# Kernel tuning notes

Measured on AMD Instinct MI355X. Metric: run time of the kernel, lower is better.

Reference implementation:

```python
import jax, jax.numpy as jnp
import numpy as np

E, N, C, A, S, H, HD, RH = 320000, 20000, 128, 4, 16, 8, 32, 64
AH = H * HD  # 256 attn-head channels; mul_alpha = AH, mul_alpha_head = HD
OUT = 128


def smooth_leaky_relu(x, a=0.2):
    # Equiformer SmoothLeakyReLU: 0.5*((1+a)*x + (1-a)*x*(2*sigmoid(x)-1))
    return 0.5 * ((1 + a) * x + (1 - a) * x * (2.0 * jax.nn.sigmoid(x) - 1.0))


def setup_inputs() -> dict:
    key = jax.random.key(0)
    ks = jax.random.split(key, 20)
    d = {
        'message': jax.random.normal(ks[0], (E, C), jnp.float32),
        'edge_attr': jax.random.normal(ks[1], (E, A), jnp.float32),
        'edge_scalars': jax.random.normal(ks[2], (E, S), jnp.float32),
        'w_rad1': jax.random.normal(ks[3], (S, RH), jnp.float32) / np.sqrt(S),
        'b_rad1': jnp.zeros((RH,), jnp.float32),
        'w_rad2': jax.random.normal(ks[4], (RH, C * A), jnp.float32) / np.sqrt(RH),
        'b_rad2': jnp.zeros((C * A,), jnp.float32),
        'w_dtp_v': jax.random.normal(ks[5], (C, A), jnp.float32) / np.sqrt(A),
        'w_lin_act': jax.random.normal(ks[6], (C, C), jnp.float32) / np.sqrt(C),
        'b_lin_act': jnp.zeros((C,), jnp.float32),
        'w_alpha': jax.random.normal(ks[7], (C, AH), jnp.float32) / np.sqrt(C),
        'b_alpha': jnp.zeros((AH,), jnp.float32),
        'w_lin_v': jax.random.normal(ks[8], (C, AH), jnp.float32) / np.sqrt(C),
        'b_lin_v': jnp.zeros((AH,), jnp.float32),
        'alpha_dot': jax.random.normal(ks[9], (H, HD), jnp.float32) / np.sqrt(HD),
        'w_proj': jax.random.normal(ks[10], (AH, OUT), jnp.float32) / np.sqrt(AH),
        'b_proj': jnp.zeros((OUT,), jnp.float32),
        'edge_dst': jax.random.randint(ks[11], (E,), 0, N, jnp.int32),
        'n_nodes_dst': N,
    }
    return d


def reference(message, edge_attr, edge_scalars,
              w_rad1, b_rad1, w_rad2, b_rad2,
              w_dtp_v, w_lin_act, b_lin_act,
              w_alpha, b_alpha, w_lin_v, b_lin_v,
              alpha_dot, w_proj, b_proj,
              edge_dst, n_nodes_dst):
    n = n_nodes_dst
    # dtp_rad: radial MLP -> per-edge depthwise TP weights [E, C, A]
    h = jax.nn.silu(edge_scalars @ w_rad1 + b_rad1)
    w = (h @ w_rad2 + b_rad2).reshape(-1, C, A)
    # sep_act.dtp (scalar irreps): out[e,c] = msg[e,c] * sum_a w[e,c,a]*attr[e,a]
    msg = message * jnp.einsum('eca,ea->ec', w, edge_attr)
    # sep_alpha -> alpha heads [E, H, HD]
    alpha = (msg @ w_alpha + b_alpha).reshape(-1, H, HD)
    # sep_act.lin + gate (scalars -> SiLU)
    value = jax.nn.silu(msg @ w_lin_act + b_lin_act)
    # sep_value: internal-weight dtp then linear, reshape to heads
    value = value * jnp.einsum('ca,ea->ec', w_dtp_v, edge_attr)
    value = (value @ w_lin_v + b_lin_v).reshape(-1, H, HD)
    # attention logits
    alpha = smooth_leaky_relu(alpha)
    alpha = jnp.einsum('ehk,hk->eh', alpha, alpha_dot)
    # scatter softmax over destination nodes
    amax = jax.ops.segment_max(alpha, edge_dst, num_segments=n)  # [N, H]
    amax = jnp.where(jnp.isfinite(amax), amax, 0.0)
    ex = jnp.exp(alpha - amax[edge_dst])
    denom = jax.ops.segment_sum(ex, edge_dst, num_segments=n)
    alpha = ex / (denom[edge_dst] + 1e-16)
    # weighted scatter-add aggregation
    attn = value * alpha[..., None]  # [E, H, HD]
    node = jax.ops.segment_sum(attn, edge_dst, num_segments=n)  # [N, H, HD]
    node = node.reshape(n, AH)  # heads2vec
    return node @ w_proj + b_proj
```

## Files before the change

kernel.cpp:

```cpp
#include <hip/hip_runtime.h>
#include <hip/hip_bf16.h>

#define C_   128
#define A_   4
#define S_   16
#define RH_  64
#define H_   8
#define AH_  256
#define OUT_ 128

typedef __attribute__((ext_vector_type(8))) short bf16x8;
typedef __attribute__((ext_vector_type(4))) float f32x4;

__device__ __forceinline__ float sigf(float x) { return 1.0f / (1.0f + __expf(-x)); }

__device__ __forceinline__ unsigned short f2bf(float x) {
    unsigned u = __float_as_uint(x);
    unsigned r = (u + 0x7fffu + ((u >> 16) & 1u)) >> 16;
    return (unsigned short)r;
}

__device__ __forceinline__ unsigned pkbf(float a, float b) {
    union { __hip_bfloat162 h; unsigned u; } c;
    c.h = __float22bfloat162_rn(float2{a, b});
    return c.u;
}

__device__ __forceinline__ unsigned enc(float x) {
    unsigned b = __float_as_uint(x);
    return (b & 0x80000000u) ? ~b : (b | 0x80000000u);
}
__device__ __forceinline__ float dec(unsigned u) {
    unsigned b = (u & 0x80000000u) ? (u & 0x7fffffffu) : ~u;
    return __uint_as_float(b);
}

__global__ void k_pack(const float* __restrict__ W, short* __restrict__ out, int K, int N) {
    const int KS = K / 32;
    const int ct = blockIdx.x / KS, ks = blockIdx.x % KS;
    const int l = threadIdx.x, lr = l & 15, lg = l >> 4;
    bf16x8 v;
    #pragma unroll
    for (int j = 0; j < 8; j++)
        v[j] = (short)f2bf(W[(size_t)(ks * 32 + lg * 8 + j) * N + ct * 16 + lr]);
    *(bf16x8*)&out[((size_t)blockIdx.x * 64 + l) * 8] = v;
}

__global__ void k_pack_dtp(const float* __restrict__ W, short* __restrict__ out) {
    const int ct = blockIdx.x >> 3, ks = blockIdx.x & 7;
    const int l = threadIdx.x, lr = l & 15, lg = l >> 4;
    bf16x8 v;
    #pragma unroll
    for (int j = 0; j < 8; j++)
        v[j] = (short)f2bf(W[(size_t)(ks * 8 + lg * 2 + (j >> 2)) * 512 + (ct * 16 + lr) * 4 + (j & 3)]);
    *(bf16x8*)&out[((size_t)blockIdx.x * 64 + l) * 8] = v;
}

__global__ __launch_bounds__(256) void k_hist(
    const int* __restrict__ edge_dst, int* __restrict__ deg, int E)
{
    const int e = blockIdx.x * 256 + threadIdx.x;
    if (e < E) atomicAdd(&deg[edge_dst[e]], 1);
}

__global__ __launch_bounds__(1024) void k_scan(
    const int* __restrict__ deg, int* __restrict__ base, int* __restrict__ cursor, int N)
{
    __shared__ int part[1024];
    const int t = threadIdx.x;
    const int per = (N + 1023) / 1024;
    const int i0 = t * per;
    int s = 0;
    for (int i = 0; i < per; i++) { int idx = i0 + i; if (idx < N) s += deg[idx]; }
    part[t] = s;
    __syncthreads();
    for (int off = 1; off < 1024; off <<= 1) {
        int v = (t >= off) ? part[t - off] : 0;
        __syncthreads();
        part[t] += v;
        __syncthreads();
    }
    int excl = (t == 0) ? 0 : part[t - 1];
    for (int i = 0; i < per; i++) {
        int idx = i0 + i;
        if (idx < N) { base[idx] = excl; cursor[idx] = excl; excl += deg[idx]; }
    }
}

__global__ __launch_bounds__(256) void k_fill(
    const int* __restrict__ edge_dst, int* __restrict__ cursor,
    int* __restrict__ sorted, int E)
{
    const int e = blockIdx.x * 256 + threadIdx.x;
    if (e < E) {
        const int pos = atomicAdd(&cursor[edge_dst[e]], 1);
        sorted[pos] = e;
    }
}

__global__ __launch_bounds__(512, 4) void k_msgalpha(
    const float* __restrict__ message, const float* __restrict__ edge_attr,
    const float* __restrict__ edge_scalars,
    const float* __restrict__ w_rad1, const float* __restrict__ b_rad1,
    const short* __restrict__ w_rad2_lin, const float* __restrict__ b_rad2,
    const short* __restrict__ w_alpha_lin, const float* __restrict__ b_alpha,
    const float* __restrict__ alpha_dot, const int* __restrict__ edge_dst,
    short* __restrict__ msg_bf, float* __restrict__ logits, unsigned* __restrict__ amax_u)
{
    __shared__ __align__(16) char smem[50432];
    short* Ap     = (short*)smem;
    short* msg_s  = (short*)(smem + 32768);
    float* w1_s   = (float*)(smem + 32768);
    float* es_s   = (float*)(smem + 32768 + 4096);
    float* attr_s = (float*)(smem + 49152);
    int*   dst_s  = (int*)(smem + 50176);

    const int t = threadIdx.x;
    const long e0 = (long)blockIdx.x * 64;

    if (t < 256) {
        *(float4*)&w1_s[t * 4] = *(const float4*)&w_rad1[t * 4];
    } else {
        const int i = t - 256, r = i >> 2, s4 = (i & 3) * 4;
        *(float4*)&es_s[r * 17 + s4] = *(const float4*)&edge_scalars[(e0 + r) * S_ + s4];
    }
    if (t < 64) {
        *(float4*)&attr_s[t * 4] = *(const float4*)&edge_attr[(e0 + t) * A_];
        dst_s[t] = edge_dst[e0 + t];
    }
    __syncthreads();

    {
        const int r = t & 63, o0 = (t >> 6) * 8;
        float acc[8];
        #pragma unroll
        for (int i = 0; i < 8; i++) acc[i] = b_rad1[o0 + i];
        #pragma unroll
        for (int s = 0; s < S_; s++) {
            const float ev = es_s[r * 17 + s];
            #pragma unroll
            for (int i = 0; i < 8; i++) acc[i] += ev * w1_s[s * 64 + o0 + i];
        }
        float h[8];
        #pragma unroll
        for (int i = 0; i < 8; i++) { const float x = acc[i]; h[i] = x * sigf(x); }
        const float4 a4 = *(const float4*)&attr_s[r * 4];
        char* base = (char*)Ap + r * 512;
        const int sw = (r & 31) << 4;
        #pragma unroll
        for (int c = 0; c < 4; c++) {
            const float h0 = h[2 * c], h1 = h[2 * c + 1];
            uint4 v;
            v.x = pkbf(h0 * a4.x, h0 * a4.y);
            v.y = pkbf(h0 * a4.z, h0 * a4.w);
            v.z = pkbf(h1 * a4.x, h1 * a4.y);
            v.w = pkbf(h1 * a4.z, h1 * a4.w);
            *(uint4*)(base + ((o0 * 8 + c * 16) ^ sw)) = v;
        }
    }
    __syncthreads();

    const int w = t >> 6, l = t & 63, lr = l & 15, lg = l >> 4;

    {
        bf16x8 bf[8];
        #pragma unroll
        for (int ks = 0; ks < 8; ks++)
            bf[ks] = *(const bf16x8*)&w_rad2_lin[((size_t)(w * 8 + ks) * 64 + l) * 8];
        const int col = w * 16 + lr;
        const float4 b2 = *(const float4*)&b_rad2[col * 4];
        #pragma unroll 1
        for (int rt = 0; rt < 4; rt++) {
            const int arow = rt * 16 + lr;
            const char* abase = (char*)Ap + arow * 512;
            const int asw = (arow & 31) << 4;
            bf16x8 af[8];
            #pragma unroll
            for (int ks = 0; ks < 8; ks++)
                af[ks] = *(const bf16x8*)(abase + ((ks * 64 + lg * 16) ^ asw));
            f32x4 acc = {0.f, 0.f, 0.f, 0.f};
            #pragma unroll
            for (int ks = 0; ks < 8; ks++)
                acc = __builtin_amdgcn_mfma_f32_16x16x32_bf16(af[ks], bf[ks], acc, 0, 0, 0);
            #pragma unroll
            for (int r = 0; r < 4; r++) {
                const int row = rt * 16 + lg * 4 + r;
                const float4 a4 = *(const float4*)&attr_s[row * 4];
                const float badj = a4.x * b2.x + a4.y * b2.y + a4.z * b2.z + a4.w * b2.w;
                const float m = message[(e0 + row) * C_ + col];
                *(short*)((char*)msg_s + row * 256 + ((col * 2) ^ ((row & 15) << 4))) =
                    (short)f2bf(m * (acc[r] + badj));
            }
        }
    }
    __syncthreads();

    {
        #pragma unroll
        for (int i = 0; i < 2; i++) {
            const int q = t + i * 512;
            const int row = q >> 4, ch = q & 15;
            const uint4 v = *(const uint4*)((char*)msg_s + row * 256 + ((ch * 16) ^ ((row & 15) << 4)));
            *(uint4*)((char*)msg_bf + ((e0 + row) * 256 + ch * 16)) = v;
        }
    }

    {
        bf16x8 waf[2][4];
        float4 ba4[2], ad4[2];
        #pragma unroll
        for (int q = 0; q < 2; q++) {
            const int rt = w * 2 + q;
            #pragma unroll
            for (int ks = 0; ks < 4; ks++)
                waf[q][ks] = *(const bf16x8*)&w_alpha_lin[((size_t)(rt * 4 + ks) * 64 + l) * 8];
            ba4[q] = *(const float4*)&b_alpha[rt * 16 + lg * 4];
            ad4[q] = *(const float4*)&alpha_dot[rt * 16 + lg * 4];
        }
        #pragma unroll 1
        for (int ct = 0; ct < 4; ct++) {
            const int erow = ct * 16 + lr;
            const char* mbase = (char*)msg_s + erow * 256;
            const int msw = (erow & 15) << 4;
            bf16x8 mb[4];
            #pragma unroll
            for (int ks = 0; ks < 4; ks++)
                mb[ks] = *(const bf16x8*)(mbase + ((ks * 64 + lg * 16) ^ msw));
            float s = 0.f;
            #pragma unroll
            for (int q = 0; q < 2; q++) {
                f32x4 acc = {0.f, 0.f, 0.f, 0.f};
                #pragma unroll
                for (int ks = 0; ks < 4; ks++)
                    acc = __builtin_amdgcn_mfma_f32_16x16x32_bf16(waf[q][ks], mb[ks], acc, 0, 0, 0);
                #pragma unroll
                for (int r = 0; r < 4; r++) {
                    const float x = acc[r] + ((const float*)&ba4[q])[r];
                    const float y = x * (0.2f + 0.8f * sigf(x));
                    s += y * ((const float*)&ad4[q])[r];
                }
            }
            s += __shfl_xor(s, 16);
            s += __shfl_xor(s, 32);
            if (lg == 0) {
                const long e = e0 + ct * 16 + lr;
                logits[e * H_ + w] = s;
                atomicMax(&amax_u[dst_s[ct * 16 + lr] * H_ + w], enc(s));
            }
        }
    }
}

__global__ __launch_bounds__(256) void k_denom(
    const float* __restrict__ logits, const int* __restrict__ edge_dst,
    const unsigned* __restrict__ amax_u, float* __restrict__ denom, int EH)
{
    const int t = blockIdx.x * 256 + threadIdx.x;
    if (t >= EH) return;
    const int e = t >> 3, h = t & 7;
    const int n = edge_dst[e];
    const float am = dec(amax_u[n * H_ + h]);
    atomicAdd(&denom[n * H_ + h], __expf(logits[t] - am));
}

__global__ __launch_bounds__(512, 2) void k_value(
    const short* __restrict__ msg_bf, const float* __restrict__ edge_attr,
    const short* __restrict__ w_lin_act_lin, const float* __restrict__ b_lin_act,
    const float* __restrict__ w_dtp_v,
    const short* __restrict__ w_lin_v_lin, const float* __restrict__ b_lin_v,
    const float* __restrict__ logits, const int* __restrict__ edge_dst,
    const unsigned* __restrict__ amax_u, const float* __restrict__ denom,
    const int* __restrict__ sorted, float* __restrict__ node)
{
    __shared__ __align__(16) char pool[66560];
    __shared__ float attr_s[64][4];
    __shared__ float wgt_s[64][H_];
    __shared__ int   dst_s[64];
    __shared__ int   eid_s[64];
    short* a_s  = (short*)pool;
    short* v_s  = (short*)(pool + 16384);
    float* val2 = (float*)pool;

    const int t = threadIdx.x;
    const int b0 = blockIdx.x * 64;

    if (t < 64) {
        const int e = sorted[b0 + t];
        eid_s[t] = e;
        dst_s[t] = edge_dst[e];
        *(float4*)&attr_s[t][0] = *(const float4*)&edge_attr[(long)e * A_];
    }
    __syncthreads();
    #pragma unroll
    for (int i = 0; i < 2; i++) {
        const int q = t + i * 512;
        const int row = q >> 4, ch = q & 15;
        const uint4 v = *(const uint4*)((const char*)msg_bf + ((long)eid_s[row] * 256 + ch * 16));
        *(uint4*)((char*)a_s + row * 256 + ((ch * 16) ^ ((row & 15) << 4))) = v;
    }
    {
        const int el = t >> 3, h = t & 7;
        const long e = eid_s[el];
        const int n = dst_s[el];
        const float am = dec(amax_u[n * H_ + h]);
        const float d  = denom[n * H_ + h];
        wgt_s[el][h] = __expf(logits[e * H_ + h] - am) / (d + 1e-16f);
    }
    __syncthreads();

    const int w = t >> 6, l = t & 63, lr = l & 15, lg = l >> 4;
    {
        bf16x8 af[4][4];
        #pragma unroll
        for (int rt = 0; rt < 4; rt++)
            #pragma unroll
            for (int ks = 0; ks < 4; ks++) {
                const int row = rt * 16 + lr;
                af[rt][ks] = *(bf16x8*)((char*)a_s + row * 256 + ((ks * 64 + lg * 16) ^ ((row & 15) << 4)));
            }
        bf16x8 bf[4];
        #pragma unroll
        for (int ks = 0; ks < 4; ks++)
            bf[ks] = *(const bf16x8*)&w_lin_act_lin[((size_t)(w * 4 + ks) * 64 + l) * 8];
        const int col = w * 16 + lr;
        const float bb = b_lin_act[col];
        const float4 wv = *(const float4*)&w_dtp_v[col * 4];
        #pragma unroll
        for (int rt = 0; rt < 4; rt++) {
            f32x4 acc = {0.f, 0.f, 0.f, 0.f};
            #pragma unroll
            for (int ks = 0; ks < 4; ks++)
                acc = __builtin_amdgcn_mfma_f32_16x16x32_bf16(af[rt][ks], bf[ks], acc, 0, 0, 0);
            #pragma unroll
            for (int r = 0; r < 4; r++) {
                const int row = rt * 16 + lg * 4 + r;
                float x = acc[r] + bb;
                x = x * sigf(x);
                const float4 a4 = *(const float4*)&attr_s[row][0];
                const float dv = wv.x * a4.x + wv.y * a4.y + wv.z * a4.z + wv.w * a4.w;
                *(short*)((char*)v_s + row * 256 + ((col * 2) ^ ((row & 15) << 4))) =
                    (short)f2bf(x * dv);
            }
        }
    }
    __syncthreads();

    bf16x8 vf[4][4];
    #pragma unroll
    for (int rt = 0; rt < 4; rt++)
        #pragma unroll
        for (int ks = 0; ks < 4; ks++) {
            const int row = rt * 16 + lr;
            vf[rt][ks] = *(bf16x8*)((char*)v_s + row * 256 + ((ks * 64 + lg * 16) ^ ((row & 15) << 4)));
        }
    __syncthreads();

    #pragma unroll
    for (int q = 0; q < 2; q++) {
        const int ct = w * 2 + q;
        bf16x8 bf[4];
        #pragma unroll
        for (int ks = 0; ks < 4; ks++)
            bf[ks] = *(const bf16x8*)&w_lin_v_lin[((size_t)(ct * 4 + ks) * 64 + l) * 8];
        const int col = ct * 16 + lr;
        const float bb = b_lin_v[col];
        #pragma unroll
        for (int rt = 0; rt < 4; rt++) {
            f32x4 acc = {0.f, 0.f, 0.f, 0.f};
            #pragma unroll
            for (int ks = 0; ks < 4; ks++)
                acc = __builtin_amdgcn_mfma_f32_16x16x32_bf16(vf[rt][ks], bf[ks], acc, 0, 0, 0);
            #pragma unroll
            for (int r = 0; r < 4; r++) {
                const int row = rt * 16 + lg * 4 + r;
                val2[row * 260 + col] = (acc[r] + bb) * wgt_s[row][col >> 5];
            }
        }
    }
    __syncthreads();
    {
        const int c = t & 255, eS = (t >> 8) * 32, eE = eS + 32;
        float run = 0.f;
        int s = eS;
        #pragma unroll 1
        for (int e = eS; e < eE; e++) {
            run += val2[e * 260 + c];
            const bool end = (e == eE - 1) || (dst_s[e + 1] != dst_s[e]);
            if (end) {
                float* np = node + (long)dst_s[e] * AH_ + c;
                if (s == eS || e == eE - 1) atomicAdd(np, run);
                else *np = run;
                run = 0.f; s = e + 1;
            }
        }
    }
}

__global__ __launch_bounds__(256) void k_proj(
    const float* __restrict__ node, const float* __restrict__ w_proj,
    const float* __restrict__ b_proj, float* __restrict__ out)
{
    __shared__ float node_s[32][AH_];
    const int t = threadIdx.x;
    const long n0 = (long)blockIdx.x * 32;
    #pragma unroll
    for (int i = 0; i < 8; i++) {
        const int idx = t + i * 256;
        const int nl = idx >> 6, c4 = (idx & 63) * 4;
        *(float4*)&node_s[nl][c4] = *(const float4*)&node[(n0 + nl) * AH_ + c4];
    }
    __syncthreads();
    const int j0 = (t & 31) * 4;
    const int g  = t >> 5;
    float4 acc4[4];
    const float4 b = *(const float4*)&b_proj[j0];
    #pragma unroll
    for (int i = 0; i < 4; i++) acc4[i] = b;
    const float* wp = w_proj + j0;
    for (int c4 = 0; c4 < 64; c4++) {
        const float4 w0 = *(const float4*)&wp[(c4 * 4 + 0) * OUT_];
        const float4 w1 = *(const float4*)&wp[(c4 * 4 + 1) * OUT_];
        const float4 w2 = *(const float4*)&wp[(c4 * 4 + 2) * OUT_];
        const float4 w3 = *(const float4*)&wp[(c4 * 4 + 3) * OUT_];
        #pragma unroll
        for (int i = 0; i < 4; i++) {
            const float4 nv = *(const float4*)&node_s[g * 4 + i][c4 * 4];
            acc4[i].x += nv.x * w0.x + nv.y * w1.x + nv.z * w2.x + nv.w * w3.x;
            acc4[i].y += nv.x * w0.y + nv.y * w1.y + nv.z * w2.y + nv.w * w3.y;
            acc4[i].z += nv.x * w0.z + nv.y * w1.z + nv.z * w2.z + nv.w * w3.z;
            acc4[i].w += nv.x * w0.w + nv.y * w1.w + nv.z * w2.w + nv.w * w3.w;
        }
    }
    #pragma unroll
    for (int i = 0; i < 4; i++) {
        const long n = n0 + g * 4 + i;
        *(float4*)&out[n * OUT_ + j0] = acc4[i];
    }
}

extern "C" void kernel_launch(void* const* d_in, const int* in_sizes, int n_in,
                              void* d_out, int out_size, void* d_ws, size_t ws_size,
                              hipStream_t stream)
{
    const float* message      = (const float*)d_in[0];
    const float* edge_attr    = (const float*)d_in[1];
    const float* edge_scalars = (const float*)d_in[2];
    const float* w_rad1       = (const float*)d_in[3];
    const float* b_rad1       = (const float*)d_in[4];
    const float* w_rad2       = (const float*)d_in[5];
    const float* b_rad2       = (const float*)d_in[6];
    const float* w_dtp_v      = (const float*)d_in[7];
    const float* w_lin_act    = (const float*)d_in[8];
    const float* b_lin_act    = (const float*)d_in[9];
    const float* w_alpha      = (const float*)d_in[10];
    const float* b_alpha      = (const float*)d_in[11];
    const float* w_lin_v      = (const float*)d_in[12];
    const float* b_lin_v      = (const float*)d_in[13];
    const float* alpha_dot    = (const float*)d_in[14];
    const float* w_proj       = (const float*)d_in[15];
    const float* b_proj       = (const float*)d_in[16];
    const int*   edge_dst     = (const int*)d_in[17];

    const int E = in_sizes[0] / C_;
    const int N = out_size / OUT_;

    char* ws = (char*)d_ws;
    float*    node     = (float*)ws;
    unsigned* amax_u   = (unsigned*)(node + (size_t)N * AH_);
    float*    denom    = (float*)(amax_u + (size_t)N * H_);
    int*      deg      = (int*)(denom + (size_t)N * H_);
    int*      base     = deg + N;
    int*      cursor   = base + N;
    int*      sorted   = cursor + N;
    short*    w_rad2_l = (short*)(sorted + E);
    short*    w_alph_l = w_rad2_l + 64 * 512;
    short*    w_lact_l = w_alph_l + 128 * 256;
    short*    w_linv_l = w_lact_l + 128 * 128;
    short*    msg_bf   = w_linv_l + 128 * 256;
    float*    logits   = (float*)(msg_bf + (size_t)E * C_);

    hipMemsetAsync(d_ws, 0, (size_t)N * (AH_ + 2 * H_ + 1) * 4, stream);

    const int nbE256 = (E + 255) / 256;
    k_pack_dtp<<<64, 64, 0, stream>>>(w_rad2, w_rad2_l);
    k_pack<<<(256/16)*(128/32), 64, 0, stream>>>(w_alpha,   w_alph_l, 128, 256);
    k_pack<<<(128/16)*(128/32), 64, 0, stream>>>(w_lin_act, w_lact_l, 128, 128);
    k_pack<<<(256/16)*(128/32), 64, 0, stream>>>(w_lin_v,   w_linv_l, 128, 256);
    k_hist<<<nbE256, 256, 0, stream>>>(edge_dst, deg, E);
    k_scan<<<1, 1024, 0, stream>>>(deg, base, cursor, N);
    k_fill<<<nbE256, 256, 0, stream>>>(edge_dst, cursor, sorted, E);
    k_msgalpha<<<E / 64, 512, 0, stream>>>(message, edge_attr, edge_scalars,
                                           w_rad1, b_rad1, w_rad2_l, b_rad2,
                                           w_alph_l, b_alpha, alpha_dot, edge_dst,
                                           msg_bf, logits, amax_u);
    k_denom<<<(E * H_ + 255) / 256, 256, 0, stream>>>(logits, edge_dst, amax_u, denom, E * H_);
    k_value<<<E / 64, 512, 0, stream>>>(msg_bf, edge_attr, w_lact_l, b_lin_act, w_dtp_v,
                                        w_linv_l, b_lin_v, logits, edge_dst, amax_u, denom,
                                        sorted, node);
    k_proj<<<N / 32, 256, 0, stream>>>(node, w_proj, b_proj, (float*)d_out);
}
```

Baseline: 420.1 us.

## Scatter msg and logit records into dst-sorted order in producer kernel

Instead of a sorted edge-index list that k_value later gathers through, k_fill now computes each edge's rank and k_msgalpha writes msg and a packed per-edge record (logits, bf16 attr, dst) straight to the sorted position. k_value then reads contiguous rows, and k_denom pre-reduces runs of equal destinations over 8 sorted edges before its atomics. k_msgalpha is also reshaped to 32 edges and 256 threads per block for higher occupancy. The cost moves to scattered writes in the producer, and edge_attr in the value path is now rounded to bf16.

```diff
diff --git a/kernel.cpp b/kernel.cpp
--- a/kernel.cpp
+++ b/kernel.cpp
@@ -25,6 +25,8 @@
     c.h = __float22bfloat162_rn(float2{a, b});
     return c.u;
 }
+__device__ __forceinline__ float bflo(unsigned u) { return __uint_as_float(u << 16); }
+__device__ __forceinline__ float bfhi(unsigned u) { return __uint_as_float(u & 0xffff0000u); }
 
 __device__ __forceinline__ unsigned enc(float x) {
     unsigned b = __float_as_uint(x);
@@ -64,7 +66,7 @@
 }
 
 __global__ __launch_bounds__(1024) void k_scan(
-    const int* __restrict__ deg, int* __restrict__ base, int* __restrict__ cursor, int N)
+    const int* __restrict__ deg, int* __restrict__ cursor, int N)
 {
     __shared__ int part[1024];
     const int t = threadIdx.x;
@@ -83,61 +85,64 @@
     int excl = (t == 0) ? 0 : part[t - 1];
     for (int i = 0; i < per; i++) {
         int idx = i0 + i;
-        if (idx < N) { base[idx] = excl; cursor[idx] = excl; excl += deg[idx]; }
+        if (idx < N) { cursor[idx] = excl; excl += deg[idx]; }
     }
 }
 
 __global__ __launch_bounds__(256) void k_fill(
     const int* __restrict__ edge_dst, int* __restrict__ cursor,
-    int* __restrict__ sorted, int E)
+    int* __restrict__ rank, int E)
 {
     const int e = blockIdx.x * 256 + threadIdx.x;
-    if (e < E) {
-        const int pos = atomicAdd(&cursor[edge_dst[e]], 1);
-        sorted[pos] = e;
-    }
-}
-
-__global__ __launch_bounds__(512, 4) void k_msgalpha(
+    if (e < E) rank[e] = atomicAdd(&cursor[edge_dst[e]], 1);
+}
+
+__global__ __launch_bounds__(256, 6) void k_msgalpha(
     const float* __restrict__ message, const float* __restrict__ edge_attr,
     const float* __restrict__ edge_scalars,
     const float* __restrict__ w_rad1, const float* __restrict__ b_rad1,
     const short* __restrict__ w_rad2_lin, const float* __restrict__ b_rad2,
     const short* __restrict__ w_alpha_lin, const float* __restrict__ b_alpha,
     const float* __restrict__ alpha_dot, const int* __restrict__ edge_dst,
-    short* __restrict__ msg_bf, float* __restrict__ logits, unsigned* __restrict__ amax_u)
-{
-    __shared__ __align__(16) char smem[50432];
+    const int* __restrict__ rank,
+    short* __restrict__ msg_srt, float* __restrict__ rec_srt, unsigned* __restrict__ amax_u)
+{
+    __shared__ __align__(16) char smem[26624];
     short* Ap     = (short*)smem;
-    short* msg_s  = (short*)(smem + 32768);
-    float* w1_s   = (float*)(smem + 32768);
-    float* es_s   = (float*)(smem + 32768 + 4096);
-    float* attr_s = (float*)(smem + 49152);
-    int*   dst_s  = (int*)(smem + 50176);
+    short* msg_s  = (short*)(smem + 16384);
+    float* w1_s   = (float*)(smem + 16384);
+    float* es_t   = (float*)(smem + 16384 + 4096);
+    float* attr_s = (float*)(smem + 24576);
+    float* rec_s  = (float*)(smem + 25088);
 
     const int t = threadIdx.x;
-    const long e0 = (long)blockIdx.x * 64;
-
-    if (t < 256) {
-        *(float4*)&w1_s[t * 4] = *(const float4*)&w_rad1[t * 4];
-    } else {
-        const int i = t - 256, r = i >> 2, s4 = (i & 3) * 4;
-        *(float4*)&es_s[r * 17 + s4] = *(const float4*)&edge_scalars[(e0 + r) * S_ + s4];
-    }
-    if (t < 64) {
-        *(float4*)&attr_s[t * 4] = *(const float4*)&edge_attr[(e0 + t) * A_];
-        dst_s[t] = edge_dst[e0 + t];
-    }
-    __syncthreads();
-
-    {
-        const int r = t & 63, o0 = (t >> 6) * 8;
+    const long e0 = (long)blockIdx.x * 32;
+
+    *(float4*)&w1_s[t * 4] = *(const float4*)&w_rad1[t * 4];
+    if (t < 128) {
+        const int r = t >> 2, s4 = (t & 3) * 4;
+        const float4 v = *(const float4*)&edge_scalars[(e0 + r) * S_ + s4];
+        es_t[(s4 + 0) * 32 + r] = v.x; es_t[(s4 + 1) * 32 + r] = v.y;
+        es_t[(s4 + 2) * 32 + r] = v.z; es_t[(s4 + 3) * 32 + r] = v.w;
+    }
+    if (t < 32) {
+        const float4 a = *(const float4*)&edge_attr[(e0 + t) * A_];
+        *(float4*)&attr_s[t * 4] = a;
+        rec_s[t * 12 + 8]  = __uint_as_float(pkbf(a.x, a.y));
+        rec_s[t * 12 + 9]  = __uint_as_float(pkbf(a.z, a.w));
+        rec_s[t * 12 + 10] = __int_as_float(edge_dst[e0 + t]);
+        rec_s[t * 12 + 11] = 0.f;
+    }
+    __syncthreads();
+
+    {
+        const int r = t & 31, o0 = (t >> 5) * 8;
         float acc[8];
         #pragma unroll
         for (int i = 0; i < 8; i++) acc[i] = b_rad1[o0 + i];
         #pragma unroll
         for (int s = 0; s < S_; s++) {
-            const float ev = es_s[r * 17 + s];
+            const float ev = es_t[s * 32 + r];
             #pragma unroll
             for (int i = 0; i < 8; i++) acc[i] += ev * w1_s[s * 64 + o0 + i];
         }
@@ -163,120 +168,143 @@
     const int w = t >> 6, l = t & 63, lr = l & 15, lg = l >> 4;
 
     {
-        bf16x8 bf[8];
-        #pragma unroll
-        for (int ks = 0; ks < 8; ks++)
-            bf[ks] = *(const bf16x8*)&w_rad2_lin[((size_t)(w * 8 + ks) * 64 + l) * 8];
-        const int col = w * 16 + lr;
-        const float4 b2 = *(const float4*)&b_rad2[col * 4];
-        #pragma unroll 1
-        for (int rt = 0; rt < 4; rt++) {
-            const int arow = rt * 16 + lr;
-            const char* abase = (char*)Ap + arow * 512;
-            const int asw = (arow & 31) << 4;
-            bf16x8 af[8];
+        #pragma unroll
+        for (int q = 0; q < 2; q++) {
+            const int ct = w * 2 + q;
+            bf16x8 bf[8];
             #pragma unroll
             for (int ks = 0; ks < 8; ks++)
-                af[ks] = *(const bf16x8*)(abase + ((ks * 64 + lg * 16) ^ asw));
-            f32x4 acc = {0.f, 0.f, 0.f, 0.f};
-            #pragma unroll
-            for (int ks = 0; ks < 8; ks++)
-                acc = __builtin_amdgcn_mfma_f32_16x16x32_bf16(af[ks], bf[ks], acc, 0, 0, 0);
-            #pragma unroll
-            for (int r = 0; r < 4; r++) {
-                const int row = rt * 16 + lg * 4 + r;
-                const float4 a4 = *(const float4*)&attr_s[row * 4];
-                const float badj = a4.x * b2.x + a4.y * b2.y + a4.z * b2.z + a4.w * b2.w;
-                const float m = message[(e0 + row) * C_ + col];
-                *(short*)((char*)msg_s + row * 256 + ((col * 2) ^ ((row & 15) << 4))) =
-                    (short)f2bf(m * (acc[r] + badj));
-            }
-        }
-    }
-    __syncthreads();
-
-    {
-        #pragma unroll
-        for (int i = 0; i < 2; i++) {
-            const int q = t + i * 512;
-            const int row = q >> 4, ch = q & 15;
-            const uint4 v = *(const uint4*)((char*)msg_s + row * 256 + ((ch * 16) ^ ((row & 15) << 4)));
-            *(uint4*)((char*)msg_bf + ((e0 + row) * 256 + ch * 16)) = v;
-        }
-    }
-
-    {
-        bf16x8 waf[2][4];
-        float4 ba4[2], ad4[2];
-        #pragma unroll
-        for (int q = 0; q < 2; q++) {
-            const int rt = w * 2 + q;
-            #pragma unroll
-            for (int ks = 0; ks < 4; ks++)
-                waf[q][ks] = *(const bf16x8*)&w_alpha_lin[((size_t)(rt * 4 + ks) * 64 + l) * 8];
-            ba4[q] = *(const float4*)&b_alpha[rt * 16 + lg * 4];
-            ad4[q] = *(const float4*)&alpha_dot[rt * 16 + lg * 4];
-        }
-        #pragma unroll 1
-        for (int ct = 0; ct < 4; ct++) {
-            const int erow = ct * 16 + lr;
-            const char* mbase = (char*)msg_s + erow * 256;
-            const int msw = (erow & 15) << 4;
-            bf16x8 mb[4];
-            #pragma unroll
-            for (int ks = 0; ks < 4; ks++)
-                mb[ks] = *(const bf16x8*)(mbase + ((ks * 64 + lg * 16) ^ msw));
-            float s = 0.f;
-            #pragma unroll
-            for (int q = 0; q < 2; q++) {
+                bf[ks] = *(const bf16x8*)&w_rad2_lin[((size_t)(ct * 8 + ks) * 64 + l) * 8];
+            const int col = ct * 16 + lr;
+            const float4 b2 = *(const float4*)&b_rad2[col * 4];
+            #pragma unroll
+            for (int rt = 0; rt < 2; rt++) {
+                const int arow = rt * 16 + lr;
+                const char* abase = (char*)Ap + arow * 512;
+                const int asw = (arow & 31) << 4;
+                bf16x8 af[8];
+                #pragma unroll
+                for (int ks = 0; ks < 8; ks++)
+                    af[ks] = *(const bf16x8*)(abase + ((ks * 64 + lg * 16) ^ asw));
                 f32x4 acc = {0.f, 0.f, 0.f, 0.f};
                 #pragma unroll
-                for (int ks = 0; ks < 4; ks++)
-                    acc = __builtin_amdgcn_mfma_f32_16x16x32_bf16(waf[q][ks], mb[ks], acc, 0, 0, 0);
+                for (int ks = 0; ks < 8; ks++)
+                    acc = __builtin_amdgcn_mfma_f32_16x16x32_bf16(af[ks], bf[ks], acc, 0, 0, 0);
                 #pragma unroll
                 for (int r = 0; r < 4; r++) {
-                    const float x = acc[r] + ((const float*)&ba4[q])[r];
-                    const float y = x * (0.2f + 0.8f * sigf(x));
-                    s += y * ((const float*)&ad4[q])[r];
+                    const int row = rt * 16 + lg * 4 + r;
+                    const float4 a4 = *(const float4*)&attr_s[row * 4];
+                    const float badj = a4.x * b2.x + a4.y * b2.y + a4.z * b2.z + a4.w * b2.w;
+                    const float m = message[(e0 + row) * C_ + col];
+                    *(short*)((char*)msg_s + row * 256 + ((col * 2) ^ ((row & 15) << 4))) =
+                        (short)f2bf(m * (acc[r] + badj));
                 }
             }
-            s += __shfl_xor(s, 16);
-            s += __shfl_xor(s, 32);
-            if (lg == 0) {
-                const long e = e0 + ct * 16 + lr;
-                logits[e * H_ + w] = s;
-                atomicMax(&amax_u[dst_s[ct * 16 + lr] * H_ + w], enc(s));
+        }
+    }
+    __syncthreads();
+
+    {
+        #pragma unroll
+        for (int i = 0; i < 2; i++) {
+            const int q = t + i * 256;
+            const int row = q >> 4, lc = q & 15;
+            const int rk = rank[e0 + row];
+            const uint4 v = *(const uint4*)((char*)msg_s + row * 256 + ((lc * 16) ^ ((row & 15) << 4)));
+            *(uint4*)((char*)msg_srt + (size_t)rk * 256 + ((lc * 16) ^ ((rk & 15) << 4))) = v;
+        }
+    }
+
+    {
+        #pragma unroll
+        for (int hq = 0; hq < 2; hq++) {
+            const int hd = w * 2 + hq;
+            bf16x8 waf[2][4];
+            float4 ba4[2], ad4[2];
+            #pragma unroll
+            for (int q = 0; q < 2; q++) {
+                const int ctw = hd * 2 + q;
+                #pragma unroll
+                for (int ks = 0; ks < 4; ks++)
+                    waf[q][ks] = *(const bf16x8*)&w_alpha_lin[((size_t)(ctw * 4 + ks) * 64 + l) * 8];
+                ba4[q] = *(const float4*)&b_alpha[ctw * 16 + lg * 4];
+                ad4[q] = *(const float4*)&alpha_dot[ctw * 16 + lg * 4];
             }
-        }
+            #pragma unroll
+            for (int ct = 0; ct < 2; ct++) {
+                const int erow = ct * 16 + lr;
+                const char* mbase = (char*)msg_s + erow * 256;
+                const int msw = (erow & 15) << 4;
+                bf16x8 mb[4];
+                #pragma unroll
+                for (int ks = 0; ks < 4; ks++)
+                    mb[ks] = *(const bf16x8*)(mbase + ((ks * 64 + lg * 16) ^ msw));
+                float s = 0.f;
+                #pragma unroll
+                for (int q = 0; q < 2; q++) {
+                    f32x4 acc = {0.f, 0.f, 0.f, 0.f};
+                    #pragma unroll
+                    for (int ks = 0; ks < 4; ks++)
+                        acc = __builtin_amdgcn_mfma_f32_16x16x32_bf16(waf[q][ks], mb[ks], acc, 0, 0, 0);
+                    #pragma unroll
+                    for (int r = 0; r < 4; r++) {
+                        const float x = acc[r] + ((const float*)&ba4[q])[r];
+                        const float y = x * (0.2f + 0.8f * sigf(x));
+                        s += y * ((const float*)&ad4[q])[r];
+                    }
+                }
+                s += __shfl_xor(s, 16);
+                s += __shfl_xor(s, 32);
+                if (lg == 0) {
+                    rec_s[(ct * 16 + lr) * 12 + hd] = s;
+                    const int n = edge_dst[e0 + ct * 16 + lr];
+                    atomicMax(&amax_u[n * H_ + hd], enc(s));
+                }
+            }
+        }
+    }
+    __syncthreads();
+
+    if (t < 96) {
+        const int e = t / 3, ch = t % 3;
+        const int rk = rank[e0 + e];
+        *(float4*)&rec_srt[(size_t)rk * 12 + ch * 4] = *(const float4*)&rec_s[e * 12 + ch * 4];
     }
 }
 
 __global__ __launch_bounds__(256) void k_denom(
-    const float* __restrict__ logits, const int* __restrict__ edge_dst,
-    const unsigned* __restrict__ amax_u, float* __restrict__ denom, int EH)
-{
-    const int t = blockIdx.x * 256 + threadIdx.x;
-    if (t >= EH) return;
-    const int e = t >> 3, h = t & 7;
-    const int n = edge_dst[e];
-    const float am = dec(amax_u[n * H_ + h]);
-    atomicAdd(&denom[n * H_ + h], __expf(logits[t] - am));
+    const float* __restrict__ rec_srt, const unsigned* __restrict__ amax_u,
+    float* __restrict__ denom, int E)
+{
+    const int idx = blockIdx.x * 256 + threadIdx.x;
+    if (idx >= E) return;
+    const int c8 = idx >> 3, h = idx & 7;
+    const float* rp = rec_srt + (size_t)c8 * 96;
+    int nprev = -1; float run = 0.f, am = 0.f;
+    #pragma unroll 1
+    for (int e = 0; e < 8; e++) {
+        const int n = __float_as_int(rp[e * 12 + 10]);
+        if (n != nprev) {
+            if (nprev >= 0) atomicAdd(&denom[nprev * H_ + h], run);
+            nprev = n; run = 0.f;
+            am = dec(amax_u[n * H_ + h]);
+        }
+        run += __expf(rp[e * 12 + h] - am);
+    }
+    atomicAdd(&denom[nprev * H_ + h], run);
 }
 
 __global__ __launch_bounds__(512, 2) void k_value(
-    const short* __restrict__ msg_bf, const float* __restrict__ edge_attr,
+    const short* __restrict__ msg_srt,
     const short* __restrict__ w_lin_act_lin, const float* __restrict__ b_lin_act,
     const float* __restrict__ w_dtp_v,
     const short* __restrict__ w_lin_v_lin, const float* __restrict__ b_lin_v,
-    const float* __restrict__ logits, const int* __restrict__ edge_dst,
-    const unsigned* __restrict__ amax_u, const float* __restrict__ denom,
-    const int* __restrict__ sorted, float* __restrict__ node)
+    const float* __restrict__ rec_srt, const unsigned* __restrict__ amax_u,
+    const float* __restrict__ denom, float* __restrict__ node)
 {
     __shared__ __align__(16) char pool[66560];
-    __shared__ float attr_s[64][4];
+    __shared__ float rec_s[64 * 12];
     __shared__ float wgt_s[64][H_];
-    __shared__ int   dst_s[64];
-    __shared__ int   eid_s[64];
     short* a_s  = (short*)pool;
     short* v_s  = (short*)(pool + 16384);
     float* val2 = (float*)pool;
@@ -284,60 +312,54 @@
     const int t = threadIdx.x;
     const int b0 = blockIdx.x * 64;
 
-    if (t < 64) {
-        const int e = sorted[b0 + t];
-        eid_s[t] = e;
-        dst_s[t] = edge_dst[e];
-        *(float4*)&attr_s[t][0] = *(const float4*)&edge_attr[(long)e * A_];
-    }
-    __syncthreads();
     #pragma unroll
     for (int i = 0; i < 2; i++) {
         const int q = t + i * 512;
-        const int row = q >> 4, ch = q & 15;
-        const uint4 v = *(const uint4*)((const char*)msg_bf + ((long)eid_s[row] * 256 + ch * 16));
-        *(uint4*)((char*)a_s + row * 256 + ((ch * 16) ^ ((row & 15) << 4))) = v;
-    }
+        *(uint4*)((char*)a_s + q * 16) =
+            *(const uint4*)((const char*)msg_srt + (size_t)b0 * 256 + q * 16);
+    }
+    if (t < 192) {
+        const int e = t / 3, ch = t % 3;
+        *(float4*)&rec_s[e * 12 + ch * 4] =
+            *(const float4*)&rec_srt[(size_t)(b0 + e) * 12 + ch * 4];
+    }
+    __syncthreads();
     {
         const int el = t >> 3, h = t & 7;
-        const long e = eid_s[el];
-        const int n = dst_s[el];
+        const int n = __float_as_int(rec_s[el * 12 + 10]);
         const float am = dec(amax_u[n * H_ + h]);
         const float d  = denom[n * H_ + h];
-        wgt_s[el][h] = __expf(logits[e * H_ + h] - am) / (d + 1e-16f);
-    }
-    __syncthreads();
+        wgt_s[el][h] = __expf(rec_s[el * 12 + h] - am) / (d + 1e-16f);
+    }
 
     const int w = t >> 6, l = t & 63, lr = l & 15, lg = l >> 4;
     {
-        bf16x8 af[4][4];
-        #pragma unroll
-        for (int rt = 0; rt < 4; rt++)
-            #pragma unroll
-            for (int ks = 0; ks < 4; ks++) {
-                const int row = rt * 16 + lr;
-                af[rt][ks] = *(bf16x8*)((char*)a_s + row * 256 + ((ks * 64 + lg * 16) ^ ((row & 15) << 4)));
-            }
-        bf16x8 bf[4];
+        bf16x8 bfg[4];
         #pragma unroll
         for (int ks = 0; ks < 4; ks++)
-            bf[ks] = *(const bf16x8*)&w_lin_act_lin[((size_t)(w * 4 + ks) * 64 + l) * 8];
+            bfg[ks] = *(const bf16x8*)&w_lin_act_lin[((size_t)(w * 4 + ks) * 64 + l) * 8];
         const int col = w * 16 + lr;
         const float bb = b_lin_act[col];
         const float4 wv = *(const float4*)&w_dtp_v[col * 4];
         #pragma unroll
         for (int rt = 0; rt < 4; rt++) {
+            const int arow = rt * 16 + lr;
+            bf16x8 af[4];
+            #pragma unroll
+            for (int ks = 0; ks < 4; ks++)
+                af[ks] = *(bf16x8*)((char*)a_s + arow * 256 + ((ks * 64 + lg * 16) ^ ((arow & 15) << 4)));
             f32x4 acc = {0.f, 0.f, 0.f, 0.f};
             #pragma unroll
             for (int ks = 0; ks < 4; ks++)
-                acc = __builtin_amdgcn_mfma_f32_16x16x32_bf16(af[rt][ks], bf[ks], acc, 0, 0, 0);
+                acc = __builtin_amdgcn_mfma_f32_16x16x32_bf16(af[ks], bfg[ks], acc, 0, 0, 0);
             #pragma unroll
             for (int r = 0; r < 4; r++) {
                 const int row = rt * 16 + lg * 4 + r;
                 float x = acc[r] + bb;
                 x = x * sigf(x);
-                const float4 a4 = *(const float4*)&attr_s[row][0];
-                const float dv = wv.x * a4.x + wv.y * a4.y + wv.z * a4.z + wv.w * a4.w;
+                const unsigned u0 = __float_as_uint(rec_s[row * 12 + 8]);
+                const unsigned u1 = __float_as_uint(rec_s[row * 12 + 9]);
+                const float dv = wv.x * bflo(u0) + wv.y * bfhi(u0) + wv.z * bflo(u1) + wv.w * bfhi(u1);
                 *(short*)((char*)v_s + row * 256 + ((col * 2) ^ ((row & 15) << 4))) =
                     (short)f2bf(x * dv);
             }
@@ -385,9 +407,10 @@
         #pragma unroll 1
         for (int e = eS; e < eE; e++) {
             run += val2[e * 260 + c];
-            const bool end = (e == eE - 1) || (dst_s[e + 1] != dst_s[e]);
+            const int de = __float_as_int(rec_s[e * 12 + 10]);
+            const bool end = (e == eE - 1) || (__float_as_int(rec_s[(e + 1) * 12 + 10]) != de);
             if (end) {
-                float* np = node + (long)dst_s[e] * AH_ + c;
+                float* np = node + (long)de * AH_ + c;
                 if (s == eS || e == eE - 1) atomicAdd(np, run);
                 else *np = run;
                 run = 0.f; s = e + 1;
@@ -469,15 +492,14 @@
     unsigned* amax_u   = (unsigned*)(node + (size_t)N * AH_);
     float*    denom    = (float*)(amax_u + (size_t)N * H_);
     int*      deg      = (int*)(denom + (size_t)N * H_);
-    int*      base     = deg + N;
-    int*      cursor   = base + N;
-    int*      sorted   = cursor + N;
-    short*    w_rad2_l = (short*)(sorted + E);
+    int*      cursor   = deg + N;
+    int*      rank     = cursor + N;
+    short*    w_rad2_l = (short*)(rank + E);
     short*    w_alph_l = w_rad2_l + 64 * 512;
     short*    w_lact_l = w_alph_l + 128 * 256;
     short*    w_linv_l = w_lact_l + 128 * 128;
-    short*    msg_bf   = w_linv_l + 128 * 256;
-    float*    logits   = (float*)(msg_bf + (size_t)E * C_);
+    short*    msg_srt  = w_linv_l + 128 * 256;
+    float*    rec_srt  = (float*)(msg_srt + (size_t)E * C_);
 
     hipMemsetAsync(d_ws, 0, (size_t)N * (AH_ + 2 * H_ + 1) * 4, stream);
 
@@ -487,15 +509,14 @@
     k_pack<<<(128/16)*(128/32), 64, 0, stream>>>(w_lin_act, w_lact_l, 128, 128);
     k_pack<<<(256/16)*(128/32), 64, 0, stream>>>(w_lin_v,   w_linv_l, 128, 256);
     k_hist<<<nbE256, 256, 0, stream>>>(edge_dst, deg, E);
-    k_scan<<<1, 1024, 0, stream>>>(deg, base, cursor, N);
-    k_fill<<<nbE256, 256, 0, stream>>>(edge_dst, cursor, sorted, E);
-    k_msgalpha<<<E / 64, 512, 0, stream>>>(message, edge_attr, edge_scalars,
+    k_scan<<<1, 1024, 0, stream>>>(deg, cursor, N);
+    k_fill<<<nbE256, 256, 0, stream>>>(edge_dst, cursor, rank, E);
+    k_msgalpha<<<E / 32, 256, 0, stream>>>(message, edge_attr, edge_scalars,
                                            w_rad1, b_rad1, w_rad2_l, b_rad2,
-                                           w_alph_l, b_alpha, alpha_dot, edge_dst,
-                                           msg_bf, logits, amax_u);
-    k_denom<<<(E * H_ + 255) / 256, 256, 0, stream>>>(logits, edge_dst, amax_u, denom, E * H_);
-    k_value<<<E / 64, 512, 0, stream>>>(msg_bf, edge_attr, w_lact_l, b_lin_act, w_dtp_v,
-                                        w_linv_l, b_lin_v, logits, edge_dst, amax_u, denom,
-                                        sorted, node);
+                                           w_alph_l, b_alpha, alpha_dot, edge_dst, rank,
+                                           msg_srt, rec_srt, amax_u);
+    k_denom<<<nbE256, 256, 0, stream>>>(rec_srt, amax_u, denom, E);
+    k_value<<<E / 64, 512, 0, stream>>>(msg_srt, w_lact_l, b_lin_act, w_dtp_v,
+                                        w_linv_l, b_lin_v, rec_srt, amax_u, denom, node);
     k_proj<<<N / 32, 256, 0, stream>>>(node, w_proj, b_proj, (float*)d_out);
 }
```

Result: slower. 543.3 us (+29.3%).

## Shrink msgalpha to 32-edge blocks of 256 threads and trim k_value register use

Applied to the files above, without the earlier changes.

k_msgalpha now processes 32 edges per block with 256 threads (4 waves), halving shared memory so more blocks fit per CU, and each wave handles two column tiles and two heads instead of one. k_value loads A fragments per row tile inside the loop instead of holding all 16 fragments in registers, lowering register pressure. The unused base array is removed from the scan. The trade-off is that B fragments of w_rad2 and w_alpha are reloaded from global memory by twice as many blocks.

```diff
diff --git a/kernel.cpp b/kernel.cpp
--- a/kernel.cpp
+++ b/kernel.cpp
@@ -64,7 +64,7 @@
 }
 
 __global__ __launch_bounds__(1024) void k_scan(
-    const int* __restrict__ deg, int* __restrict__ base, int* __restrict__ cursor, int N)
+    const int* __restrict__ deg, int* __restrict__ cursor, int N)
 {
     __shared__ int part[1024];
     const int t = threadIdx.x;
@@ -83,7 +83,7 @@
     int excl = (t == 0) ? 0 : part[t - 1];
     for (int i = 0; i < per; i++) {
         int idx = i0 + i;
-        if (idx < N) { base[idx] = excl; cursor[idx] = excl; excl += deg[idx]; }
+        if (idx < N) { cursor[idx] = excl; excl += deg[idx]; }
     }
 }
 
@@ -98,7 +98,7 @@
     }
 }
 
-__global__ __launch_bounds__(512, 4) void k_msgalpha(
+__global__ __launch_bounds__(256, 6) void k_msgalpha(
     const float* __restrict__ message, const float* __restrict__ edge_attr,
     const float* __restrict__ edge_scalars,
     const float* __restrict__ w_rad1, const float* __restrict__ b_rad1,
@@ -107,31 +107,30 @@
     const float* __restrict__ alpha_dot, const int* __restrict__ edge_dst,
     short* __restrict__ msg_bf, float* __restrict__ logits, unsigned* __restrict__ amax_u)
 {
-    __shared__ __align__(16) char smem[50432];
+    __shared__ __align__(16) char smem[25216];
     short* Ap     = (short*)smem;
-    short* msg_s  = (short*)(smem + 32768);
-    float* w1_s   = (float*)(smem + 32768);
-    float* es_s   = (float*)(smem + 32768 + 4096);
-    float* attr_s = (float*)(smem + 49152);
-    int*   dst_s  = (int*)(smem + 50176);
+    short* msg_s  = (short*)(smem + 16384);
+    float* w1_s   = (float*)(smem + 16384);
+    float* es_s   = (float*)(smem + 16384 + 4096);
+    float* attr_s = (float*)(smem + 24576);
+    int*   dst_s  = (int*)(smem + 25088);
 
     const int t = threadIdx.x;
-    const long e0 = (long)blockIdx.x * 64;
-
-    if (t < 256) {
-        *(float4*)&w1_s[t * 4] = *(const float4*)&w_rad1[t * 4];
-    } else {
-        const int i = t - 256, r = i >> 2, s4 = (i & 3) * 4;
+    const long e0 = (long)blockIdx.x * 32;
+
+    *(float4*)&w1_s[t * 4] = *(const float4*)&w_rad1[t * 4];
+    if (t < 128) {
+        const int r = t >> 2, s4 = (t & 3) * 4;
         *(float4*)&es_s[r * 17 + s4] = *(const float4*)&edge_scalars[(e0 + r) * S_ + s4];
     }
-    if (t < 64) {
+    if (t < 32) {
         *(float4*)&attr_s[t * 4] = *(const float4*)&edge_attr[(e0 + t) * A_];
         dst_s[t] = edge_dst[e0 + t];
     }
     __syncthreads();
 
     {
-        const int r = t & 63, o0 = (t >> 6) * 8;
+        const int r = t & 31, o0 = (t >> 5) * 8;
         float acc[8];
         #pragma unroll
         for (int i = 0; i < 8; i++) acc[i] = b_rad1[o0 + i];
@@ -163,33 +162,37 @@
     const int w = t >> 6, l = t & 63, lr = l & 15, lg = l >> 4;
 
     {
-        bf16x8 bf[8];
-        #pragma unroll
-        for (int ks = 0; ks < 8; ks++)
-            bf[ks] = *(const bf16x8*)&w_rad2_lin[((size_t)(w * 8 + ks) * 64 + l) * 8];
-        const int col = w * 16 + lr;
-        const float4 b2 = *(const float4*)&b_rad2[col * 4];
-        #pragma unroll 1
-        for (int rt = 0; rt < 4; rt++) {
-            const int arow = rt * 16 + lr;
-            const char* abase = (char*)Ap + arow * 512;
-            const int asw = (arow & 31) << 4;
-            bf16x8 af[8];
+        #pragma unroll
+        for (int q = 0; q < 2; q++) {
+            const int ct = w * 2 + q;
+            bf16x8 bf[8];
             #pragma unroll
             for (int ks = 0; ks < 8; ks++)
-                af[ks] = *(const bf16x8*)(abase + ((ks * 64 + lg * 16) ^ asw));
-            f32x4 acc = {0.f, 0.f, 0.f, 0.f};
-            #pragma unroll
-            for (int ks = 0; ks < 8; ks++)
-                acc = __builtin_amdgcn_mfma_f32_16x16x32_bf16(af[ks], bf[ks], acc, 0, 0, 0);
-            #pragma unroll
-            for (int r = 0; r < 4; r++) {
-                const int row = rt * 16 + lg * 4 + r;
-                const float4 a4 = *(const float4*)&attr_s[row * 4];
-                const float badj = a4.x * b2.x + a4.y * b2.y + a4.z * b2.z + a4.w * b2.w;
-                const float m = message[(e0 + row) * C_ + col];
-                *(short*)((char*)msg_s + row * 256 + ((col * 2) ^ ((row & 15) << 4))) =
-                    (short)f2bf(m * (acc[r] + badj));
+                bf[ks] = *(const bf16x8*)&w_rad2_lin[((size_t)(ct * 8 + ks) * 64 + l) * 8];
+            const int col = ct * 16 + lr;
+            const float4 b2 = *(const float4*)&b_rad2[col * 4];
+            #pragma unroll
+            for (int rt = 0; rt < 2; rt++) {
+                const int arow = rt * 16 + lr;
+                const char* abase = (char*)Ap + arow * 512;
+                const int asw = (arow & 31) << 4;
+                bf16x8 af[8];
+                #pragma unroll
+                for (int ks = 0; ks < 8; ks++)
+                    af[ks] = *(const bf16x8*)(abase + ((ks * 64 + lg * 16) ^ asw));
+                f32x4 acc = {0.f, 0.f, 0.f, 0.f};
+                #pragma unroll
+                for (int ks = 0; ks < 8; ks++)
+                    acc = __builtin_amdgcn_mfma_f32_16x16x32_bf16(af[ks], bf[ks], acc, 0, 0, 0);
+                #pragma unroll
+                for (int r = 0; r < 4; r++) {
+                    const int row = rt * 16 + lg * 4 + r;
+                    const float4 a4 = *(const float4*)&attr_s[row * 4];
+                    const float badj = a4.x * b2.x + a4.y * b2.y + a4.z * b2.z + a4.w * b2.w;
+                    const float m = message[(e0 + row) * C_ + col];
+                    *(short*)((char*)msg_s + row * 256 + ((col * 2) ^ ((row & 15) << 4))) =
+                        (short)f2bf(m * (acc[r] + badj));
+                }
             }
         }
     }
@@ -198,7 +201,7 @@
     {
         #pragma unroll
         for (int i = 0; i < 2; i++) {
-            const int q = t + i * 512;
+            const int q = t + i * 256;
             const int row = q >> 4, ch = q & 15;
             const uint4 v = *(const uint4*)((char*)msg_s + row * 256 + ((ch * 16) ^ ((row & 15) << 4)));
             *(uint4*)((char*)msg_bf + ((e0 + row) * 256 + ch * 16)) = v;
@@ -206,46 +209,50 @@
     }
 
     {
-        bf16x8 waf[2][4];
-        float4 ba4[2], ad4[2];
-        #pragma unroll
-        for (int q = 0; q < 2; q++) {
-            const int rt = w * 2 + q;
-            #pragma unroll
-            for (int ks = 0; ks < 4; ks++)
-                waf[q][ks] = *(const bf16x8*)&w_alpha_lin[((size_t)(rt * 4 + ks) * 64 + l) * 8];
-            ba4[q] = *(const float4*)&b_alpha[rt * 16 + lg * 4];
-            ad4[q] = *(const float4*)&alpha_dot[rt * 16 + lg * 4];
-        }
-        #pragma unroll 1
-        for (int ct = 0; ct < 4; ct++) {
-            const int erow = ct * 16 + lr;
-            const char* mbase = (char*)msg_s + erow * 256;
-            const int msw = (erow & 15) << 4;
-            bf16x8 mb[4];
-            #pragma unroll
-            for (int ks = 0; ks < 4; ks++)
-                mb[ks] = *(const bf16x8*)(mbase + ((ks * 64 + lg * 16) ^ msw));
-            float s = 0.f;
+        #pragma unroll
+        for (int hq = 0; hq < 2; hq++) {
+            const int hd = w * 2 + hq;
+            bf16x8 waf[2][4];
+            float4 ba4[2], ad4[2];
             #pragma unroll
             for (int q = 0; q < 2; q++) {
-                f32x4 acc = {0.f, 0.f, 0.f, 0.f};
+                const int ctw = hd * 2 + q;
                 #pragma unroll
                 for (int ks = 0; ks < 4; ks++)
-                    acc = __builtin_amdgcn_mfma_f32_16x16x32_bf16(waf[q][ks], mb[ks], acc, 0, 0, 0);
+                    waf[q][ks] = *(const bf16x8*)&w_alpha_lin[((size_t)(ctw * 4 + ks) * 64 + l) * 8];
+                ba4[q] = *(const float4*)&b_alpha[ctw * 16 + lg * 4];
+                ad4[q] = *(const float4*)&alpha_dot[ctw * 16 + lg * 4];
+            }
+            #pragma unroll
+            for (int ct = 0; ct < 2; ct++) {
+                const int erow = ct * 16 + lr;
+                const char* mbase = (char*)msg_s + erow * 256;
+                const int msw = (erow & 15) << 4;
+                bf16x8 mb[4];
                 #pragma unroll
-                for (int r = 0; r < 4; r++) {
-                    const float x = acc[r] + ((const float*)&ba4[q])[r];
-                    const float y = x * (0.2f + 0.8f * sigf(x));
-                    s += y * ((const float*)&ad4[q])[r];
+                for (int ks = 0; ks < 4; ks++)
+                    mb[ks] = *(const bf16x8*)(mbase + ((ks * 64 + lg * 16) ^ msw));
+                float s = 0.f;
+                #pragma unroll
+                for (int q = 0; q < 2; q++) {
+                    f32x4 acc = {0.f, 0.f, 0.f, 0.f};
+                    #pragma unroll
+                    for (int ks = 0; ks < 4; ks++)
+                        acc = __builtin_amdgcn_mfma_f32_16x16x32_bf16(waf[q][ks], mb[ks], acc, 0, 0, 0);
+                    #pragma unroll
+                    for (int r = 0; r < 4; r++) {
+                        const float x = acc[r] + ((const float*)&ba4[q])[r];
+                        const float y = x * (0.2f + 0.8f * sigf(x));
+                        s += y * ((const float*)&ad4[q])[r];
+                    }
                 }
-            }
-            s += __shfl_xor(s, 16);
-            s += __shfl_xor(s, 32);
-            if (lg == 0) {
-                const long e = e0 + ct * 16 + lr;
-                logits[e * H_ + w] = s;
-                atomicMax(&amax_u[dst_s[ct * 16 + lr] * H_ + w], enc(s));
+                s += __shfl_xor(s, 16);
+                s += __shfl_xor(s, 32);
+                if (lg == 0) {
+                    const long e = e0 + ct * 16 + lr;
+                    logits[e * H_ + hd] = s;
+                    atomicMax(&amax_u[dst_s[ct * 16 + lr] * H_ + hd], enc(s));
+                }
             }
         }
     }
@@ -310,27 +317,24 @@
 
     const int w = t >> 6, l = t & 63, lr = l & 15, lg = l >> 4;
     {
-        bf16x8 af[4][4];
-        #pragma unroll
-        for (int rt = 0; rt < 4; rt++)
-            #pragma unroll
-            for (int ks = 0; ks < 4; ks++) {
-                const int row = rt * 16 + lr;
-                af[rt][ks] = *(bf16x8*)((char*)a_s + row * 256 + ((ks * 64 + lg * 16) ^ ((row & 15) << 4)));
-            }
-        bf16x8 bf[4];
+        bf16x8 bfg[4];
         #pragma unroll
         for (int ks = 0; ks < 4; ks++)
-            bf[ks] = *(const bf16x8*)&w_lin_act_lin[((size_t)(w * 4 + ks) * 64 + l) * 8];
+            bfg[ks] = *(const bf16x8*)&w_lin_act_lin[((size_t)(w * 4 + ks) * 64 + l) * 8];
         const int col = w * 16 + lr;
         const float bb = b_lin_act[col];
         const float4 wv = *(const float4*)&w_dtp_v[col * 4];
         #pragma unroll
         for (int rt = 0; rt < 4; rt++) {
+            const int arow = rt * 16 + lr;
+            bf16x8 af[4];
+            #pragma unroll
+            for (int ks = 0; ks < 4; ks++)
+                af[ks] = *(bf16x8*)((char*)a_s + arow * 256 + ((ks * 64 + lg * 16) ^ ((arow & 15) << 4)));
             f32x4 acc = {0.f, 0.f, 0.f, 0.f};
             #pragma unroll
             for (int ks = 0; ks < 4; ks++)
-                acc = __builtin_amdgcn_mfma_f32_16x16x32_bf16(af[rt][ks], bf[ks], acc, 0, 0, 0);
+                acc = __builtin_amdgcn_mfma_f32_16x16x32_bf16(af[ks], bfg[ks], acc, 0, 0, 0);
             #pragma unroll
             for (int r = 0; r < 4; r++) {
                 const int row = rt * 16 + lg * 4 + r;
@@ -469,8 +473,7 @@
     unsigned* amax_u   = (unsigned*)(node + (size_t)N * AH_);
     float*    denom    = (float*)(amax_u + (size_t)N * H_);
     int*      deg      = (int*)(denom + (size_t)N * H_);
-    int*      base     = deg + N;
-    int*      cursor   = base + N;
+    int*      cursor   = deg + N;
     int*      sorted   = cursor + N;
     short*    w_rad2_l = (short*)(sorted + E);
     short*    w_alph_l = w_rad2_l + 64 * 512;
@@ -487,9 +490,9 @@
     k_pack<<<(128/16)*(128/32), 64, 0, stream>>>(w_lin_act, w_lact_l, 128, 128);
     k_pack<<<(256/16)*(128/32), 64, 0, stream>>>(w_lin_v,   w_linv_l, 128, 256);
     k_hist<<<nbE256, 256, 0, stream>>>(edge_dst, deg, E);
-    k_scan<<<1, 1024, 0, stream>>>(deg, base, cursor, N);
+    k_scan<<<1, 1024, 0, stream>>>(deg, cursor, N);
     k_fill<<<nbE256, 256, 0, stream>>>(edge_dst, cursor, sorted, E);
-    k_msgalpha<<<E / 64, 512, 0, stream>>>(message, edge_attr, edge_scalars,
+    k_msgalpha<<<E / 32, 256, 0, stream>>>(message, edge_attr, edge_scalars,
                                            w_rad1, b_rad1, w_rad2_l, b_rad2,
                                            w_alph_l, b_alpha, alpha_dot, edge_dst,
                                            msg_bf, logits, amax_u);
```

New measurement: 558.0 us. 32.8% more time.
